# Kernel tuning notes

Hardware: AMD Instinct MI355X
Metric: run time of the kernel (lower is better)

## Reference

```python
import jax, jax.numpy as jnp
import numpy as np

FT_IN = 64 * (10 * 64 + 1)   # 41024
K_HALF = 256
FT_OUT = 2 * K_HALF          # 512
B = 8192


def clip01(x):
    return jnp.clip(x, 0.0, 1.0)


def setup_inputs() -> dict:
    key = jax.random.key(0)
    ks = jax.random.split(key, 10)
    # note: torch init zeros ft weight/bias; we use random params so the
    # reference exercises real data flow (zeros would hide bugs).
    s_ft = 1.0 / np.sqrt(FT_IN)
    s_h1 = 1.0 / np.sqrt(FT_OUT)
    s_h2 = 1.0 / np.sqrt(32)
    return {
        "features1": jax.random.uniform(ks[0], (B, FT_IN), dtype=jnp.float32),
        "features2": jax.random.uniform(ks[1], (B, FT_IN), dtype=jnp.float32),
        "ft_w": jax.random.uniform(ks[2], (K_HALF, FT_IN), jnp.float32, -s_ft, s_ft),
        "ft_b": jax.random.uniform(ks[3], (K_HALF,), jnp.float32, -s_ft, s_ft),
        "h1_w": jax.random.uniform(ks[4], (32, FT_OUT), jnp.float32, -s_h1, s_h1),
        "h1_b": jax.random.uniform(ks[5], (32,), jnp.float32, -s_h1, s_h1),
        "h2_w": jax.random.uniform(ks[6], (32, 32), jnp.float32, -s_h2, s_h2),
        "h2_b": jax.random.uniform(ks[7], (32,), jnp.float32, -s_h2, s_h2),
        "out_w": jax.random.uniform(ks[8], (1, 32), jnp.float32, -s_h2, s_h2),
        "out_b": jax.random.uniform(ks[9], (1,), jnp.float32, -s_h2, s_h2),
    }


def reference(features1, features2, ft_w, ft_b, h1_w, h1_b, h2_w, h2_b, out_w, out_b):
    # feature transform applied to both perspectives, then concat  -> [B, 512]
    f1 = features1 @ ft_w.T + ft_b
    f2 = features2 @ ft_w.T + ft_b
    ft_out = clip01(jnp.concatenate([f1, f2], axis=1))
    h1 = clip01(ft_out @ h1_w.T + h1_b)   # [B, 32]
    h2 = clip01(h1 @ h2_w.T + h2_b)       # [B, 32]
    return h2 @ out_w.T + out_b           # [B, 1]
```

## Files before the change

kernel.cpp:

```cpp
#include <hip/hip_runtime.h>
#include <stdint.h>
#include <stddef.h>

#define FT_IN 41024
#define KHALF 256
#define BATCH 8192
#define NKT 641

typedef __attribute__((ext_vector_type(8))) short short8;
typedef __attribute__((ext_vector_type(4))) short short4v;
typedef __attribute__((ext_vector_type(4))) float f32x4;
typedef __attribute__((ext_vector_type(2))) uint32_t u32x2;
typedef __attribute__((ext_vector_type(4))) _Float16 half4v;

typedef const __attribute__((address_space(1))) uint32_t* gas1_t;
typedef __attribute__((address_space(3))) uint32_t* las3_t;

__device__ __forceinline__ unsigned short f2bf(float f) {
  union { float f; uint32_t u; } x; x.f = f;
  uint32_t u = x.u + 0x7FFFu + ((x.u >> 16) & 1u);
  return (unsigned short)(u >> 16);
}

#define MFMA16(acc, a, b) \
  asm("v_mfma_f32_16x16x32_bf16 %0, %1, %2, %0" : "+v"(acc) : "v"(a), "v"(b))

#define CVTPK(dst, lo, hi) \
  asm("v_cvt_pk_bf16_f32 %0, %1, %2" : "=v"(dst) : "v"(lo), "v"(hi))

__global__ void wprep_kernel(const float* __restrict__ w,
                             unsigned short* __restrict__ o, int n4) {
  int i = blockIdx.x * blockDim.x + threadIdx.x;
  int stride = gridDim.x * blockDim.x;
  for (; i < n4; i += stride) {
    f32x4 v = ((const f32x4*)w)[i];
    short4v b;
    b.x = (short)f2bf(v.x); b.y = (short)f2bf(v.y);
    b.z = (short)f2bf(v.z); b.w = (short)f2bf(v.w);
    ((short4v*)o)[i] = b;
  }
}

__global__ __launch_bounds__(256, 2) void ftgemm_kernel(
    const float* __restrict__ f1g, const float* __restrict__ f2g,
    const unsigned short* __restrict__ wb,
    _Float16* __restrict__ part, int KS) {
  __shared__ alignas(16) char sA[16384];
  __shared__ alignas(16) char sW[2][32768];

  const int nwg = (int)gridDim.x;
  const int orig = (int)blockIdx.x;
  int bid = (orig & 7) * (nwg >> 3) + (orig >> 3);

  const int rb = bid & 63; bid >>= 6;
  const int st = bid & 1;  bid >>= 1;
  const int ks = bid;

  const int kt0 = (ks * NKT) / KS;
  const int kt1 = ((ks + 1) * NKT) / KS;

  const int tid  = (int)threadIdx.x;
  const int lane = tid & 63;
  const int wv   = tid >> 6;
  const int wr   = (wv >> 1) << 6;
  const int wc   = (wv & 1) << 7;
  const int r16  = lane & 15;
  const int hi   = lane >> 4;

  const float* F = (st ? f2g : f1g) + (size_t)rb * (128ull * FT_IN);

  const int arow = tid >> 4;
  const int akc  = tid & 15;
  const float* aptr = F + (size_t)arow * FT_IN + (size_t)kt0 * 64 + akc * 4;

  const int wrow = tid >> 3;
  const int wkc  = tid & 7;
  const int wkcs = wkc ^ (wrow & 7);
  const unsigned short* wptr =
      wb + (size_t)wrow * FT_IN + (size_t)kt0 * 64;

  f32x4 areg[8];
  f32x4 acc[4][8];
  const f32x4 fzero = {0.f, 0.f, 0.f, 0.f};
  #pragma unroll
  for (int m = 0; m < 4; ++m)
    #pragma unroll
    for (int n = 0; n < 8; ++n) acc[m][n] = fzero;

  #pragma unroll
  for (int i = 0; i < 8; ++i)
    areg[i] = *(const f32x4*)(aptr + (size_t)i * (16ull * FT_IN));
  #pragma unroll
  for (int i = 0; i < 8; ++i) {
    const unsigned short* g = wptr + (size_t)i * (32ull * FT_IN) + wkcs * 8;
    __builtin_amdgcn_global_load_lds((gas1_t)g,
        (las3_t)&sW[0][(i * 256 + tid) * 16], 16, 0, 0);
  }

  int buf = 0;
  for (int kt = kt0; kt < kt1; ++kt) {
    #pragma unroll
    for (int i = 0; i < 8; ++i) {
      const int row = i * 16 + arow;
      f32x4 v = areg[i];
      uint32_t b0, b1;
      CVTPK(b0, v.x, v.y);
      CVTPK(b1, v.z, v.w);
      u32x2 b; b.x = b0; b.y = b1;
      *(u32x2*)(sA + row * 128 + ((akc * 8) ^ ((row & 7) << 4))) = b;
    }
    __syncthreads();

    if (kt + 1 < kt1) {
      const int d = kt + 1 - kt0;
      const float* ap = aptr + d * 64;
      #pragma unroll
      for (int i = 0; i < 8; ++i)
        areg[i] = *(const f32x4*)(ap + (size_t)i * (16ull * FT_IN));
      const unsigned short* wp = wptr + d * 64;
      #pragma unroll
      for (int i = 0; i < 8; ++i) {
        const unsigned short* g = wp + (size_t)i * (32ull * FT_IN) + wkcs * 8;
        __builtin_amdgcn_global_load_lds((gas1_t)g,
            (las3_t)&sW[buf ^ 1][(i * 256 + tid) * 16], 16, 0, 0);
      }
    }

    const char* sWb = sW[buf];
    const int swz = (r16 & 7) << 4;
    #pragma unroll
    for (int k2 = 0; k2 < 2; ++k2) {
      const int ko = (k2 * 64 + hi * 16) ^ swz;
      short8 av[4], bv[8];
      #pragma unroll
      for (int m = 0; m < 4; ++m)
        av[m] = *(const short8*)(sA + (wr + m * 16 + r16) * 128 + ko);
      #pragma unroll
      for (int n = 0; n < 8; ++n)
        bv[n] = *(const short8*)(sWb + (wc + n * 16 + r16) * 128 + ko);
      #pragma unroll
      for (int m = 0; m < 4; ++m)
        #pragma unroll
        for (int n = 0; n < 8; ++n)
          MFMA16(acc[m][n], av[m], bv[n]);
    }

    __builtin_amdgcn_sched_barrier(0);
    __builtin_amdgcn_s_barrier();
    __builtin_amdgcn_sched_barrier(0);
    buf ^= 1;
  }

  _Float16* pb = part + (size_t)(ks * 2 + st) * (KHALF * (size_t)BATCH);
  const int growb = rb * 128 + wr + hi * 4;
  const int gcolb = wc + r16;
  #pragma unroll
  for (int n = 0; n < 8; ++n)
    #pragma unroll
    for (int m = 0; m < 4; ++m) {
      f32x4 a = acc[m][n];
      half4v h;
      h.x = (_Float16)a.x; h.y = (_Float16)a.y;
      h.z = (_Float16)a.z; h.w = (_Float16)a.w;
      *(half4v*)(pb + (size_t)(gcolb + n * 16) * BATCH + (growb + m * 16)) = h;
    }
}

__global__ __launch_bounds__(256) void tail_kernel(
    const _Float16* __restrict__ part,
    const float* __restrict__ ftb, const float* __restrict__ h1w,
    const float* __restrict__ h1b, const float* __restrict__ h2w,
    const float* __restrict__ h2b, const float* __restrict__ outw,
    const float* __restrict__ outb, float* __restrict__ out, int KS) {
  __shared__ float sh1t[512 * 36];
  __shared__ float sh2[32 * 32];
  __shared__ float sow[32];
  __shared__ float sh1b[32];
  __shared__ float sh2b[32];
  __shared__ float sftb[256];
  __shared__ float sob[1];

  const int tid = (int)threadIdx.x;
  for (int i = tid; i < 512 * 32; i += 256) {
    const int j = i >> 9, c = i & 511;
    sh1t[c * 36 + j] = h1w[i];
  }
  for (int i = tid; i < 1024; i += 256) sh2[i] = h2w[i];
  if (tid < 32) { sow[tid] = outw[tid]; sh1b[tid] = h1b[tid]; sh2b[tid] = h2b[tid]; }
  sftb[tid] = ftb[tid];
  if (tid == 0) sob[0] = outb[0];
  __syncthreads();

  const int r  = tid & 31;
  const int cg = tid >> 5;
  const int t  = (int)blockIdx.x * 32 + r;

  float a1p[32];
  #pragma unroll
  for (int j = 0; j < 32; ++j) a1p[j] = 0.f;

  for (int ci = 0; ci < 64; ++ci) {
    const int c   = cg * 64 + ci;
    const int set = c >> 8;
    const int cs  = c & 255;
    float v = sftb[cs];
    const _Float16* p = part + ((size_t)set * KHALF + cs) * BATCH + t;
    for (int kq = 0; kq < KS; ++kq)
      v += (float)p[(size_t)kq * (2ull * KHALF * BATCH)];
    v = fminf(fmaxf(v, 0.f), 1.f);
    const f32x4* wr4 = (const f32x4*)(sh1t + c * 36);
    #pragma unroll
    for (int q = 0; q < 8; ++q) {
      f32x4 wv = wr4[q];
      a1p[q * 4 + 0] += v * wv.x; a1p[q * 4 + 1] += v * wv.y;
      a1p[q * 4 + 2] += v * wv.z; a1p[q * 4 + 3] += v * wv.w;
    }
  }

  float* red = sh1t;
  __syncthreads();
  #pragma unroll
  for (int j = 0; j < 32; ++j)
    red[(cg * 32 + r) * 33 + j] = a1p[j];
  __syncthreads();

  if (tid < 32) {
    float a1[32];
    #pragma unroll
    for (int j = 0; j < 32; ++j) a1[j] = sh1b[j];
    for (int g = 0; g < 8; ++g)
      #pragma unroll
      for (int j = 0; j < 32; ++j)
        a1[j] += red[(g * 32 + tid) * 33 + j];
    #pragma unroll
    for (int j = 0; j < 32; ++j) a1[j] = fminf(fmaxf(a1[j], 0.f), 1.f);

    float a2[32];
    #pragma unroll
    for (int j = 0; j < 32; ++j) {
      float x = sh2b[j];
      const f32x4* w2 = (const f32x4*)(sh2 + j * 32);
      #pragma unroll
      for (int q = 0; q < 8; ++q) {
        f32x4 wv = w2[q];
        x += a1[q * 4 + 0] * wv.x + a1[q * 4 + 1] * wv.y +
             a1[q * 4 + 2] * wv.z + a1[q * 4 + 3] * wv.w;
      }
      a2[j] = fminf(fmaxf(x, 0.f), 1.f);
    }
    float o = sob[0];
    #pragma unroll
    for (int j = 0; j < 32; ++j) o += a2[j] * sow[j];
    out[(int)blockIdx.x * 32 + tid] = o;
  }
}

extern "C" void kernel_launch(void* const* d_in, const int* in_sizes, int n_in,
                              void* d_out, int out_size, void* d_ws, size_t ws_size,
                              hipStream_t stream) {
  const float* f1   = (const float*)d_in[0];
  const float* f2   = (const float*)d_in[1];
  const float* ftw  = (const float*)d_in[2];
  const float* ftb  = (const float*)d_in[3];
  const float* h1w  = (const float*)d_in[4];
  const float* h1b  = (const float*)d_in[5];
  const float* h2w  = (const float*)d_in[6];
  const float* h2b  = (const float*)d_in[7];
  const float* outw = (const float*)d_in[8];
  const float* outb = (const float*)d_in[9];
  float* out = (float*)d_out;

  unsigned short* wb = (unsigned short*)d_ws;
  const size_t woff = (size_t)KHALF * FT_IN * 2;
  _Float16* part = (_Float16*)((char*)d_ws + woff);
  const size_t per = 2ull * KHALF * BATCH * 2;

  int KS = 1;
  if (ws_size >= woff + 4 * per)      KS = 4;
  else if (ws_size >= woff + 2 * per) KS = 2;

  wprep_kernel<<<2048, 256, 0, stream>>>(ftw, wb, (KHALF * FT_IN) / 4);
  ftgemm_kernel<<<dim3(64 * 2 * KS), 256, 0, stream>>>(f1, f2, wb, part, KS);
  tail_kernel<<<BATCH / 32, 256, 0, stream>>>(part, ftb, h1w, h1b, h2w, h2b,
                                              outw, outb, out, KS);
}
```

Before: 653.5 us.

## Drop K-split; use 32-row full-K tiles with fused bias/clip epilogue

Replaces the K-split GEMM with 128-row tiles by full-K blocks covering 32 batch rows and all 256 output columns. Activations are staged in 256-wide macro chunks with weights streamed per 64-wide subtile. Bias and clip are applied in the GEMM epilogue, removing the partial-sum buffer and reduction in the tail kernel. It trades far more weight re-reads and smaller per-wave MFMA tiles for contiguous activation reads and no partial traffic.

```diff
diff --git a/kernel.cpp b/kernel.cpp
--- a/kernel.cpp
+++ b/kernel.cpp
@@ -5,7 +5,7 @@
 #define FT_IN 41024
 #define KHALF 256
 #define BATCH 8192
-#define NKT 641
+#define NMACRO 160
 
 typedef __attribute__((ext_vector_type(8))) short short8;
 typedef __attribute__((ext_vector_type(4))) short short4v;
@@ -44,52 +44,50 @@
 __global__ __launch_bounds__(256, 2) void ftgemm_kernel(
     const float* __restrict__ f1g, const float* __restrict__ f2g,
     const unsigned short* __restrict__ wb,
-    _Float16* __restrict__ part, int KS) {
+    const float* __restrict__ ftbv,
+    _Float16* __restrict__ ftout) {
   __shared__ alignas(16) char sA[16384];
   __shared__ alignas(16) char sW[2][32768];
 
   const int nwg = (int)gridDim.x;
   const int orig = (int)blockIdx.x;
   int bid = (orig & 7) * (nwg >> 3) + (orig >> 3);
-
-  const int rb = bid & 63; bid >>= 6;
-  const int st = bid & 1;  bid >>= 1;
-  const int ks = bid;
-
-  const int kt0 = (ks * NKT) / KS;
-  const int kt1 = ((ks + 1) * NKT) / KS;
+  const int rb = bid & 255;
+  const int st = bid >> 8;
 
   const int tid  = (int)threadIdx.x;
   const int lane = tid & 63;
   const int wv   = tid >> 6;
-  const int wr   = (wv >> 1) << 6;
-  const int wc   = (wv & 1) << 7;
+  const int wc   = wv << 6;
   const int r16  = lane & 15;
   const int hi   = lane >> 4;
 
-  const float* F = (st ? f2g : f1g) + (size_t)rb * (128ull * FT_IN);
-
-  const int arow = tid >> 4;
-  const int akc  = tid & 15;
-  const float* aptr = F + (size_t)arow * FT_IN + (size_t)kt0 * 64 + akc * 4;
+  const float* F = (st ? f2g : f1g) + (size_t)rb * (32ull * FT_IN);
+
+  const int arow = tid >> 3;
+  const int achk = tid & 7;
+  const float* aptr = F + (size_t)arow * FT_IN + achk * 32;
 
   const int wrow = tid >> 3;
   const int wkc  = tid & 7;
   const int wkcs = wkc ^ (wrow & 7);
-  const unsigned short* wptr =
-      wb + (size_t)wrow * FT_IN + (size_t)kt0 * 64;
+  const unsigned short* wptr = wb + (size_t)wrow * FT_IN;
+
+  float fb[4];
+  #pragma unroll
+  for (int n = 0; n < 4; ++n) fb[n] = ftbv[wc + n * 16 + r16];
 
   f32x4 areg[8];
-  f32x4 acc[4][8];
+  f32x4 acc[2][4];
   const f32x4 fzero = {0.f, 0.f, 0.f, 0.f};
   #pragma unroll
-  for (int m = 0; m < 4; ++m)
-    #pragma unroll
-    for (int n = 0; n < 8; ++n) acc[m][n] = fzero;
+  for (int m = 0; m < 2; ++m)
+    #pragma unroll
+    for (int n = 0; n < 4; ++n) acc[m][n] = fzero;
 
   #pragma unroll
   for (int i = 0; i < 8; ++i)
-    areg[i] = *(const f32x4*)(aptr + (size_t)i * (16ull * FT_IN));
+    areg[i] = *(const f32x4*)(aptr + i * 4);
   #pragma unroll
   for (int i = 0; i < 8; ++i) {
     const unsigned short* g = wptr + (size_t)i * (32ull * FT_IN) + wkcs * 8;
@@ -97,87 +95,112 @@
         (las3_t)&sW[0][(i * 256 + tid) * 16], 16, 0, 0);
   }
 
+  const int xr = (arow & 7) << 4;
+  const int swz = (r16 & 7) << 4;
   int buf = 0;
-  for (int kt = kt0; kt < kt1; ++kt) {
-    #pragma unroll
-    for (int i = 0; i < 8; ++i) {
-      const int row = i * 16 + arow;
-      f32x4 v = areg[i];
-      uint32_t b0, b1;
-      CVTPK(b0, v.x, v.y);
-      CVTPK(b1, v.z, v.w);
-      u32x2 b; b.x = b0; b.y = b1;
-      *(u32x2*)(sA + row * 128 + ((akc * 8) ^ ((row & 7) << 4))) = b;
-    }
-    __syncthreads();
-
-    if (kt + 1 < kt1) {
-      const int d = kt + 1 - kt0;
-      const float* ap = aptr + d * 64;
-      #pragma unroll
-      for (int i = 0; i < 8; ++i)
-        areg[i] = *(const f32x4*)(ap + (size_t)i * (16ull * FT_IN));
-      const unsigned short* wp = wptr + d * 64;
+
+  for (int mt = 0; mt <= NMACRO; ++mt) {
+    const bool lastm = (mt == NMACRO);
+    if (!lastm) {
       #pragma unroll
       for (int i = 0; i < 8; ++i) {
-        const unsigned short* g = wp + (size_t)i * (32ull * FT_IN) + wkcs * 8;
-        __builtin_amdgcn_global_load_lds((gas1_t)g,
-            (las3_t)&sW[buf ^ 1][(i * 256 + tid) * 16], 16, 0, 0);
-      }
-    }
-
-    const char* sWb = sW[buf];
-    const int swz = (r16 & 7) << 4;
-    #pragma unroll
-    for (int k2 = 0; k2 < 2; ++k2) {
-      const int ko = (k2 * 64 + hi * 16) ^ swz;
-      short8 av[4], bv[8];
-      #pragma unroll
-      for (int m = 0; m < 4; ++m)
-        av[m] = *(const short8*)(sA + (wr + m * 16 + r16) * 128 + ko);
-      #pragma unroll
-      for (int n = 0; n < 8; ++n)
-        bv[n] = *(const short8*)(sWb + (wc + n * 16 + r16) * 128 + ko);
-      #pragma unroll
-      for (int m = 0; m < 4; ++m)
-        #pragma unroll
-        for (int n = 0; n < 8; ++n)
-          MFMA16(acc[m][n], av[m], bv[n]);
-    }
-
+        f32x4 v = areg[i];
+        uint32_t b0, b1;
+        CVTPK(b0, v.x, v.y);
+        CVTPK(b1, v.z, v.w);
+        u32x2 b; b.x = b0; b.y = b1;
+        *(u32x2*)(sA + arow * 512 + ((achk * 64 + i * 8) ^ xr)) = b;
+      }
+    } else {
+      #pragma unroll
+      for (int i = 0; i < 2; ++i) {
+        f32x4 v = areg[i];
+        uint32_t b0, b1;
+        CVTPK(b0, v.x, v.y);
+        CVTPK(b1, v.z, v.w);
+        u32x2 b; b.x = b0; b.y = b1;
+        *(u32x2*)(sA + arow * 512 + ((achk * 16 + i * 8) ^ xr)) = b;
+      }
+    }
+    const int nsub = lastm ? 1 : 4;
+    for (int s2 = 0; s2 < nsub; ++s2) {
+      __syncthreads();
+      const int gs = mt * 4 + s2;
+      if (gs < 640) {
+        const unsigned short* wp = wptr + (size_t)(gs + 1) * 64;
+        #pragma unroll
+        for (int i = 0; i < 8; ++i) {
+          const unsigned short* g = wp + (size_t)i * (32ull * FT_IN) + wkcs * 8;
+          __builtin_amdgcn_global_load_lds((gas1_t)g,
+              (las3_t)&sW[buf ^ 1][(i * 256 + tid) * 16], 16, 0, 0);
+        }
+      }
+      if (!lastm && s2 == 3) {
+        if (mt + 1 < NMACRO) {
+          const float* ap = aptr + (size_t)(mt + 1) * 256;
+          #pragma unroll
+          for (int i = 0; i < 8; ++i)
+            areg[i] = *(const f32x4*)(ap + i * 4);
+        } else {
+          const float* ap = F + (size_t)arow * FT_IN + NMACRO * 256 + achk * 8;
+          areg[0] = *(const f32x4*)(ap);
+          areg[1] = *(const f32x4*)(ap + 4);
+        }
+      }
+      const char* sWb = sW[buf];
+      #pragma unroll
+      for (int k2 = 0; k2 < 2; ++k2) {
+        const int koA = (s2 * 128 + k2 * 64 + hi * 16) ^ swz;
+        const int koW = (k2 * 64 + hi * 16) ^ swz;
+        short8 av[2], bv[4];
+        #pragma unroll
+        for (int m = 0; m < 2; ++m)
+          av[m] = *(const short8*)(sA + (m * 16 + r16) * 512 + koA);
+        #pragma unroll
+        for (int n = 0; n < 4; ++n)
+          bv[n] = *(const short8*)(sWb + (wc + n * 16 + r16) * 128 + koW);
+        #pragma unroll
+        for (int m = 0; m < 2; ++m)
+          #pragma unroll
+          for (int n = 0; n < 4; ++n)
+            MFMA16(acc[m][n], av[m], bv[n]);
+      }
+      buf ^= 1;
+    }
     __builtin_amdgcn_sched_barrier(0);
     __builtin_amdgcn_s_barrier();
     __builtin_amdgcn_sched_barrier(0);
-    buf ^= 1;
-  }
-
-  _Float16* pb = part + (size_t)(ks * 2 + st) * (KHALF * (size_t)BATCH);
-  const int growb = rb * 128 + wr + hi * 4;
-  const int gcolb = wc + r16;
-  #pragma unroll
-  for (int n = 0; n < 8; ++n)
-    #pragma unroll
-    for (int m = 0; m < 4; ++m) {
+  }
+
+  _Float16* pb = ftout + (size_t)(st * KHALF) * BATCH;
+  const int growb = rb * 32 + hi * 4;
+  #pragma unroll
+  for (int n = 0; n < 4; ++n) {
+    const int gcol = wc + n * 16 + r16;
+    #pragma unroll
+    for (int m = 0; m < 2; ++m) {
       f32x4 a = acc[m][n];
       half4v h;
-      h.x = (_Float16)a.x; h.y = (_Float16)a.y;
-      h.z = (_Float16)a.z; h.w = (_Float16)a.w;
-      *(half4v*)(pb + (size_t)(gcolb + n * 16) * BATCH + (growb + m * 16)) = h;
-    }
+      h.x = (_Float16)fminf(fmaxf(a.x + fb[n], 0.f), 1.f);
+      h.y = (_Float16)fminf(fmaxf(a.y + fb[n], 0.f), 1.f);
+      h.z = (_Float16)fminf(fmaxf(a.z + fb[n], 0.f), 1.f);
+      h.w = (_Float16)fminf(fmaxf(a.w + fb[n], 0.f), 1.f);
+      *(half4v*)(pb + (size_t)gcol * BATCH + (growb + m * 16)) = h;
+    }
+  }
 }
 
 __global__ __launch_bounds__(256) void tail_kernel(
-    const _Float16* __restrict__ part,
-    const float* __restrict__ ftb, const float* __restrict__ h1w,
-    const float* __restrict__ h1b, const float* __restrict__ h2w,
-    const float* __restrict__ h2b, const float* __restrict__ outw,
-    const float* __restrict__ outb, float* __restrict__ out, int KS) {
+    const _Float16* __restrict__ ft,
+    const float* __restrict__ h1w, const float* __restrict__ h1b,
+    const float* __restrict__ h2w, const float* __restrict__ h2b,
+    const float* __restrict__ outw, const float* __restrict__ outb,
+    float* __restrict__ out) {
   __shared__ float sh1t[512 * 36];
   __shared__ float sh2[32 * 32];
   __shared__ float sow[32];
   __shared__ float sh1b[32];
   __shared__ float sh2b[32];
-  __shared__ float sftb[256];
   __shared__ float sob[1];
 
   const int tid = (int)threadIdx.x;
@@ -187,7 +210,6 @@
   }
   for (int i = tid; i < 1024; i += 256) sh2[i] = h2w[i];
   if (tid < 32) { sow[tid] = outw[tid]; sh1b[tid] = h1b[tid]; sh2b[tid] = h2b[tid]; }
-  sftb[tid] = ftb[tid];
   if (tid == 0) sob[0] = outb[0];
   __syncthreads();
 
@@ -200,14 +222,8 @@
   for (int j = 0; j < 32; ++j) a1p[j] = 0.f;
 
   for (int ci = 0; ci < 64; ++ci) {
-    const int c   = cg * 64 + ci;
-    const int set = c >> 8;
-    const int cs  = c & 255;
-    float v = sftb[cs];
-    const _Float16* p = part + ((size_t)set * KHALF + cs) * BATCH + t;
-    for (int kq = 0; kq < KS; ++kq)
-      v += (float)p[(size_t)kq * (2ull * KHALF * BATCH)];
-    v = fminf(fmaxf(v, 0.f), 1.f);
+    const int c = cg * 64 + ci;
+    float v = (float)ft[(size_t)c * BATCH + t];
     const f32x4* wr4 = (const f32x4*)(sh1t + c * 36);
     #pragma unroll
     for (int q = 0; q < 8; ++q) {
@@ -272,15 +288,10 @@
 
   unsigned short* wb = (unsigned short*)d_ws;
   const size_t woff = (size_t)KHALF * FT_IN * 2;
-  _Float16* part = (_Float16*)((char*)d_ws + woff);
-  const size_t per = 2ull * KHALF * BATCH * 2;
-
-  int KS = 1;
-  if (ws_size >= woff + 4 * per)      KS = 4;
-  else if (ws_size >= woff + 2 * per) KS = 2;
+  _Float16* ftbuf = (_Float16*)((char*)d_ws + woff);
 
   wprep_kernel<<<2048, 256, 0, stream>>>(ftw, wb, (KHALF * FT_IN) / 4);
-  ftgemm_kernel<<<dim3(64 * 2 * KS), 256, 0, stream>>>(f1, f2, wb, part, KS);
-  tail_kernel<<<BATCH / 32, 256, 0, stream>>>(part, ftb, h1w, h1b, h2w, h2b,
-                                              outw, outb, out, KS);
-}
+  ftgemm_kernel<<<512, 256, 0, stream>>>(f1, f2, wb, ftb, ftbuf);
+  tail_kernel<<<BATCH / 32, 256, 0, stream>>>(ftbuf, h1w, h1b, h2w, h2b,
+                                              outw, outb, out);
+}
```

Measured after the change: 1.182 ms. +80.9%, slower.
